# Kernel optimization log

Hardware: AMD Instinct MI355X
Metric: run time of the kernel (lower is better)

The kernel has to match this reference:

```python
import jax, jax.numpy as jnp
import numpy as np

N = 50000          # nodes
E = 400000         # edges
F = 128            # num_embeddings
NUM_TYPES = 100    # num_atoms (embedding vocab)
CUTOFF = 5.0
N_RBF = 20


def _silu(x):
    return x * jax.nn.sigmoid(x)


def setup_inputs() -> dict:
    key = jax.random.key(0)
    ks = jax.random.split(key, 16)
    pos = jax.random.normal(ks[0], (N, 3), dtype=jnp.float32) * 3.0
    z = jax.random.randint(ks[1], (N,), 0, NUM_TYPES)
    dst = jax.random.randint(ks[2], (E,), 0, N)
    # ensure src != dst so distances are nonzero
    src = (dst + 1 + jax.random.randint(ks[3], (E,), 0, N - 1)) % N
    def lin(k, fan_in, fan_out):
        kw, kb = jax.random.split(k)
        lim = 1.0 / np.sqrt(fan_in)
        W = jax.random.uniform(kw, (fan_out, fan_in), minval=-lim, maxval=lim, dtype=jnp.float32)
        b = jax.random.uniform(kb, (fan_out,), minval=-lim, maxval=lim, dtype=jnp.float32)
        return W, b
    emb_table = jax.random.normal(ks[4], (NUM_TYPES, F), dtype=jnp.float32)
    Wp1, bp1 = lin(ks[5], F, F)
    Wp2, bp2 = lin(ks[6], F, 3 * F)
    Ww, bw = lin(ks[7], N_RBF, 3 * F)
    Wu, bu = lin(ks[8], F, F)
    Wv, bv = lin(ks[9], F, F)
    Wu1, bu1 = lin(ks[10], 2 * F, F)
    Wu2, bu2 = lin(ks[11], F, 3 * F)
    return dict(pos=pos, emb_table=emb_table,
                Wp1=Wp1, bp1=bp1, Wp2=Wp2, bp2=bp2, Ww=Ww, bw=bw,
                Wu=Wu, bu=bu, Wv=Wv, bv=bv, Wu1=Wu1, bu1=bu1, Wu2=Wu2, bu2=bu2,
                z=z, src=src, dst=dst)


def painn_forward(pos, emb_table, Wp1, bp1, Wp2, bp2, Ww, bw, Wu, bu, Wv, bv,
                  Wu1, bu1, Wu2, bu2, z, src, dst):
    s = emb_table[z]                                  # [N,F] scalar features
    v = jnp.zeros((N, F, 3), dtype=s.dtype)          # equivariant features

    # ---- message block ----
    phi = _silu(s @ Wp1.T + bp1) @ Wp2.T + bp2       # [N,3F]
    rel = pos[dst] - pos[src]                        # [E,3]
    d = jnp.maximum(jnp.linalg.norm(rel, axis=-1), 1e-9)  # [E]
    n = jnp.arange(1, N_RBF + 1, dtype=jnp.float32)
    rbf = jnp.sin(n * jnp.pi * d[:, None] / CUTOFF) / d[:, None]   # [E,20]
    Wf = rbf @ Ww.T + bw                             # [E,3F]
    split = phi[src] * Wf                            # [E,3F] gated message
    ds = jax.ops.segment_sum(split[:, :F], dst, num_segments=N)    # [N,F]
    direction = rel / d[:, None]                     # [E,3]
    dv_e = v[src] * split[:, F:2 * F, None] + split[:, 2 * F:, None] * direction[:, None, :]  # [E,F,3]
    dv = jax.ops.segment_sum(dv_e, dst, num_segments=N)            # [N,F,3]
    s = s + ds
    v = v + dv

    # ---- update block ----
    U = jnp.einsum('nfc,gf->ngc', v, Wu) + bu[:, None]   # [N,F,3]
    V = jnp.einsum('nfc,gf->ngc', v, Wv) + bv[:, None]   # [N,F,3]
    Vn = jnp.linalg.norm(V, axis=-1)                     # [N,F]
    h = jnp.concatenate([s, Vn], axis=-1)                # [N,2F]
    a = _silu(h @ Wu1.T + bu1) @ Wu2.T + bu2             # [N,3F]
    dv2 = U * a[:, :F, None]                             # [N,F,3]
    ds2 = a[:, F:2 * F] + jnp.sum(U * V, axis=-1) * a[:, 2 * F:]   # [N,F]
    return s + ds2, v + dv2


def reference(pos, emb_table, Wp1, bp1, Wp2, bp2, Ww, bw, Wu, bu, Wv, bv,
              Wu1, bu1, Wu2, bu2, z, src, dst):
    return painn_forward(pos, emb_table, Wp1, bp1, Wp2, bp2, Ww, bw, Wu, bu,
                         Wv, bv, Wu1, bu1, Wu2, bu2, z, src, dst)
```

## Files before the change

kernel.cpp:

```cpp
#include <hip/hip_runtime.h>

#define NN 50000
#define EE 400000
#define FF 128
#define NRBF 20
#define MAXDEG 64
#define PI_OVER_CUT 0.6283185307179586f

typedef _Float16 h8 __attribute__((ext_vector_type(8)));
typedef float    f4 __attribute__((ext_vector_type(4)));

__global__ __launch_bounds__(256) void k_zero(int* __restrict__ counts) {
    int i = blockIdx.x * 256 + threadIdx.x;
    if (i < NN) counts[i] = 0;
}

__global__ __launch_bounds__(256) void k_bucket(const int* __restrict__ dst,
                                                int* __restrict__ counts,
                                                int* __restrict__ slots) {
    int e = blockIdx.x * 256 + threadIdx.x;
    if (e < EE) {
        int n = dst[e];
        int slot = atomicAdd(&counts[n], 1);
        if (slot < MAXDEG) slots[n * MAXDEG + slot] = e;
    }
}

__global__ __launch_bounds__(256) void k_wconv(
    const float* __restrict__ Wu, const float* __restrict__ Wv,
    const float* __restrict__ Wu1, const float* __restrict__ Wu2,
    const float* __restrict__ Wp1, const float* __restrict__ Wp2,
    _Float16* __restrict__ Wuh, _Float16* __restrict__ Wvh,
    _Float16* __restrict__ Wu1h, _Float16* __restrict__ Wu2h,
    _Float16* __restrict__ Wp1h, _Float16* __restrict__ Wp2h)
{
    int i = blockIdx.x * 256 + threadIdx.x;
    if (i < 16384) { Wuh[i] = (_Float16)Wu[i]; Wvh[i] = (_Float16)Wv[i];
                     Wp1h[i] = (_Float16)Wp1[i]; }
    if (i < 32768) { Wu1h[i] = (_Float16)Wu1[i]; }
    if (i < 49152) { Wu2h[i] = (_Float16)Wu2[i]; Wp2h[i] = (_Float16)Wp2[i]; }
}

__global__ __launch_bounds__(256) void k_node_phi_mfma(
    const float* __restrict__ emb, const int* __restrict__ z,
    const _Float16* __restrict__ Wp1h, const float* __restrict__ bp1,
    const _Float16* __restrict__ Wp2h, const float* __restrict__ bp2,
    _Float16* __restrict__ phi_s, _Float16* __restrict__ phi_v,
    float* __restrict__ s_io)
{
    __shared__ _Float16 Ss[32 * 128];
    __shared__ _Float16 H1s[32 * 128];

    const int t    = threadIdx.x;
    const int lane = t & 63;
    const int w    = t >> 6;
    const int lr   = lane & 15;
    const int lq   = lane >> 4;
    const int n0   = blockIdx.x * 32;
    const f4 z4 = {0.f, 0.f, 0.f, 0.f};

    for (int i = t; i < 512; i += 256) {
        int n = i >> 4, gr = i & 15;
        int nn = n0 + n; if (nn > NN - 1) nn = NN - 1;
        const float* sp = &emb[(size_t)z[nn] * FF + gr * 8];
        float4 aa = *(const float4*)sp;
        float4 bb = *(const float4*)(sp + 4);
        h8 hv;
        hv[0] = (_Float16)aa.x; hv[1] = (_Float16)aa.y;
        hv[2] = (_Float16)aa.z; hv[3] = (_Float16)aa.w;
        hv[4] = (_Float16)bb.x; hv[5] = (_Float16)bb.y;
        hv[6] = (_Float16)bb.z; hv[7] = (_Float16)bb.w;
        *(h8*)&Ss[(n * 16 + (gr ^ (n & 15))) * 8] = hv;
        float* op = &s_io[(size_t)nn * FF + gr * 8];
        *(float4*)op       = aa;
        *(float4*)(op + 4) = bb;
    }
    __syncthreads();

    f4 acc1[2][2];
    #pragma unroll
    for (int a = 0; a < 2; ++a)
        #pragma unroll
        for (int m = 0; m < 2; ++m) acc1[a][m] = z4;
    {
        const _Float16* bb = Wp1h + (size_t)lr * 128 + lq * 8;
        #pragma unroll
        for (int g2 = 0; g2 < 2; ++g2) {
            h8 bf[4];
            #pragma unroll
            for (int ks = 0; ks < 4; ++ks)
                bf[ks] = *(const h8*)(bb + ((2 * w + g2) * 16) * 128 + ks * 32);
            #pragma unroll
            for (int mt = 0; mt < 2; ++mt) {
                const int r = mt * 16 + lr;
                #pragma unroll
                for (int ks = 0; ks < 4; ++ks) {
                    h8 af = *(const h8*)&Ss[(r * 16 + ((ks * 4 + lq) ^ (r & 15))) * 8];
                    acc1[g2][mt] = __builtin_amdgcn_mfma_f32_16x16x32_f16(
                        af, bf[ks], acc1[g2][mt], 0, 0, 0);
                }
            }
        }
    }
    #pragma unroll
    for (int g2 = 0; g2 < 2; ++g2) {
        const int g = (2 * w + g2) * 16 + lr;
        const float b1 = bp1[g];
        #pragma unroll
        for (int mt = 0; mt < 2; ++mt)
            #pragma unroll
            for (int r = 0; r < 4; ++r) {
                float x = acc1[g2][mt][r] + b1;
                float y = x / (1.f + __expf(-x));
                int n = mt * 16 + lq * 4 + r;
                H1s[(n * 16 + ((g >> 3) ^ (n & 15))) * 8 + (g & 7)] = (_Float16)y;
            }
    }
    __syncthreads();

    f4 accS[2][2], accV[2][2];
    #pragma unroll
    for (int a = 0; a < 2; ++a)
        #pragma unroll
        for (int m = 0; m < 2; ++m) { accS[a][m] = z4; accV[a][m] = z4; }
    {
        const _Float16* bbs = Wp2h + (size_t)lr * 128 + lq * 8;
        const _Float16* bbv = Wp2h + (size_t)(256 + lr) * 128 + lq * 8;
        #pragma unroll
        for (int g2 = 0; g2 < 2; ++g2) {
            h8 bfs[4], bfv[4];
            #pragma unroll
            for (int ks = 0; ks < 4; ++ks) {
                bfs[ks] = *(const h8*)(bbs + ((2 * w + g2) * 16) * 128 + ks * 32);
                bfv[ks] = *(const h8*)(bbv + ((2 * w + g2) * 16) * 128 + ks * 32);
            }
            #pragma unroll
            for (int mt = 0; mt < 2; ++mt) {
                const int r = mt * 16 + lr;
                #pragma unroll
                for (int ks = 0; ks < 4; ++ks) {
                    h8 af = *(const h8*)&H1s[(r * 16 + ((ks * 4 + lq) ^ (r & 15))) * 8];
                    accS[g2][mt] = __builtin_amdgcn_mfma_f32_16x16x32_f16(
                        af, bfs[ks], accS[g2][mt], 0, 0, 0);
                    accV[g2][mt] = __builtin_amdgcn_mfma_f32_16x16x32_f16(
                        af, bfv[ks], accV[g2][mt], 0, 0, 0);
                }
            }
        }
    }
    #pragma unroll
    for (int g2 = 0; g2 < 2; ++g2) {
        const int g = (2 * w + g2) * 16 + lr;
        const float bsa = bp2[g], bva = bp2[256 + g];
        #pragma unroll
        for (int mt = 0; mt < 2; ++mt)
            #pragma unroll
            for (int r = 0; r < 4; ++r) {
                int n = mt * 16 + lq * 4 + r;
                int nn = n0 + n;
                if (nn < NN) {
                    size_t gi = (size_t)nn * FF + g;
                    phi_s[gi] = (_Float16)(accS[g2][mt][r] + bsa);
                    phi_v[gi] = (_Float16)(accV[g2][mt][r] + bva);
                }
            }
    }
}

__global__ __launch_bounds__(128) void k_edge(
    const float* __restrict__ pos,
    const float* __restrict__ Ww, const float* __restrict__ bw,
    const int* __restrict__ src,
    const int* __restrict__ counts, const int* __restrict__ slots,
    const _Float16* __restrict__ phi_s, const _Float16* __restrict__ phi_v,
    float* __restrict__ s_io, float* __restrict__ v_io,
    _Float16* __restrict__ xg)
{
    const int n = blockIdx.x;
    const int f = threadIdx.x;
    const int lane = threadIdx.x & 63;

    float ww_s[NRBF], ww_v[NRBF];
    #pragma unroll
    for (int k = 0; k < NRBF; k++) {
        ww_s[k] = Ww[f * NRBF + k];
        ww_v[k] = Ww[(256 + f) * NRBF + k];
    }
    const float bws = bw[f], bwv = bw[256 + f];
    const float px = pos[3 * n], py = pos[3 * n + 1], pz = pos[3 * n + 2];

    float acc_s = 0.f, av0 = 0.f, av1 = 0.f, av2 = 0.f;
    int deg = counts[n];
    deg = deg > MAXDEG ? MAXDEG : deg;

    for (int i = 0; i < deg; i++) {
        int e  = slots[n * MAXDEG + i];
        int sI = src[e];
        float rx = px - pos[3 * sI];
        float ry = py - pos[3 * sI + 1];
        float rz = pz - pos[3 * sI + 2];
        float d = sqrtf(rx * rx + ry * ry + rz * rz);
        d = fmaxf(d, 1e-9f);
        float dinv = 1.f / d;
        int kk = lane < NRBF ? lane : (NRBF - 1);
        float rbf_l = __sinf((float)(kk + 1) * PI_OVER_CUT * d) * dinv;
        int rbf_i = __float_as_int(rbf_l);
        float wfs = bws, wfv = bwv;
        #pragma unroll
        for (int k = 0; k < NRBF; k++) {
            float rk = __int_as_float(__builtin_amdgcn_readlane(rbf_i, k));
            wfs = fmaf(ww_s[k], rk, wfs);
            wfv = fmaf(ww_v[k], rk, wfv);
        }
        float sp_s = (float)phi_s[(size_t)sI * FF + f] * wfs;
        float sp_v = (float)phi_v[(size_t)sI * FF + f] * wfv;
        acc_s += sp_s;
        av0 = fmaf(sp_v, rx * dinv, av0);
        av1 = fmaf(sp_v, ry * dinv, av1);
        av2 = fmaf(sp_v, rz * dinv, av2);
    }
    size_t gi = (size_t)n * FF + f;
    s_io[gi] += acc_s;
    v_io[gi * 3 + 0] = av0;
    v_io[gi * 3 + 1] = av1;
    v_io[gi * 3 + 2] = av2;
    xg[((size_t)n * 3 + 0) * FF + f] = (_Float16)av0;
    xg[((size_t)n * 3 + 1) * FF + f] = (_Float16)av1;
    xg[((size_t)n * 3 + 2) * FF + f] = (_Float16)av2;
}

__global__ __launch_bounds__(256) void k_update_mfma(
    const _Float16* __restrict__ xg,
    const _Float16* __restrict__ Wuh, const _Float16* __restrict__ Wvh,
    const _Float16* __restrict__ Wu1h, const _Float16* __restrict__ Wu2h,
    const float* __restrict__ bu, const float* __restrict__ bv,
    const float* __restrict__ bu1, const float* __restrict__ bu2,
    float* __restrict__ s_io, float* __restrict__ v_io)
{
    __shared__ _Float16 Xs[96 * 128];
    __shared__ _Float16 Hs[32 * 256];
    __shared__ _Float16 H1s[32 * 128];

    const int t    = threadIdx.x;
    const int lane = t & 63;
    const int w    = t >> 6;
    const int lr   = lane & 15;
    const int lq   = lane >> 4;
    const int n0   = blockIdx.x * 32;
    const f4 z4 = {0.f, 0.f, 0.f, 0.f};

    for (int i = t; i < 1536; i += 256) {
        int row = i >> 4, gr = i & 15;
        int n = row & 31, c = row >> 5;
        int nn = n0 + n; if (nn > NN - 1) nn = NN - 1;
        uint4 d = *(const uint4*)&xg[((size_t)nn * 3 + c) * FF + gr * 8];
        *(uint4*)&Xs[(row * 16 + (gr ^ (row & 15))) * 8] = d;
    }
    for (int i = t; i < 512; i += 256) {
        int n = i >> 4, gr = i & 15;
        int nn = n0 + n; if (nn > NN - 1) nn = NN - 1;
        const float* sp = &s_io[(size_t)nn * FF + gr * 8];
        float4 aa = *(const float4*)sp;
        float4 bb = *(const float4*)(sp + 4);
        h8 hv;
        hv[0] = (_Float16)aa.x; hv[1] = (_Float16)aa.y;
        hv[2] = (_Float16)aa.z; hv[3] = (_Float16)aa.w;
        hv[4] = (_Float16)bb.x; hv[5] = (_Float16)bb.y;
        hv[6] = (_Float16)bb.z; hv[7] = (_Float16)bb.w;
        *(h8*)&Hs[(n * 32 + (gr ^ (n & 15))) * 8] = hv;
    }
    __syncthreads();

    f4 accU[2][6], accV[2][6];
    #pragma unroll
    for (int a = 0; a < 2; ++a)
        #pragma unroll
        for (int m = 0; m < 6; ++m) { accU[a][m] = z4; accV[a][m] = z4; }

    {
        const _Float16* bb = Wuh + (size_t)lr * 128 + lq * 8;
        h8 bf[2][4];
        #pragma unroll
        for (int g2 = 0; g2 < 2; ++g2)
            #pragma unroll
            for (int ks = 0; ks < 4; ++ks)
                bf[g2][ks] = *(const h8*)(bb + ((2 * w + g2) * 16) * 128 + ks * 32);
        #pragma unroll
        for (int mt = 0; mt < 6; ++mt) {
            const int r = mt * 16 + lr;
            h8 af[4];
            #pragma unroll
            for (int ks = 0; ks < 4; ++ks)
                af[ks] = *(const h8*)&Xs[(r * 16 + ((ks * 4 + lq) ^ (r & 15))) * 8];
            #pragma unroll
            for (int g2 = 0; g2 < 2; ++g2)
                #pragma unroll
                for (int ks = 0; ks < 4; ++ks)
                    accU[g2][mt] = __builtin_amdgcn_mfma_f32_16x16x32_f16(
                        af[ks], bf[g2][ks], accU[g2][mt], 0, 0, 0);
        }
    }
    {
        const _Float16* bb = Wvh + (size_t)lr * 128 + lq * 8;
        h8 bf[2][4];
        #pragma unroll
        for (int g2 = 0; g2 < 2; ++g2)
            #pragma unroll
            for (int ks = 0; ks < 4; ++ks)
                bf[g2][ks] = *(const h8*)(bb + ((2 * w + g2) * 16) * 128 + ks * 32);
        #pragma unroll
        for (int mt = 0; mt < 6; ++mt) {
            const int r = mt * 16 + lr;
            h8 af[4];
            #pragma unroll
            for (int ks = 0; ks < 4; ++ks)
                af[ks] = *(const h8*)&Xs[(r * 16 + ((ks * 4 + lq) ^ (r & 15))) * 8];
            #pragma unroll
            for (int g2 = 0; g2 < 2; ++g2)
                #pragma unroll
                for (int ks = 0; ks < 4; ++ks)
                    accV[g2][mt] = __builtin_amdgcn_mfma_f32_16x16x32_f16(
                        af[ks], bf[g2][ks], accV[g2][mt], 0, 0, 0);
        }
    }

    float uvr[2][2][4];
    #pragma unroll
    for (int g2 = 0; g2 < 2; ++g2) {
        const int g = (2 * w + g2) * 16 + lr;
        const float bU = bu[g], bV = bv[g];
        #pragma unroll
        for (int p = 0; p < 2; ++p) {
            #pragma unroll
            for (int r = 0; r < 4; ++r) {
                float Ux = accU[g2][0 + p][r] + bU;
                float Uy = accU[g2][2 + p][r] + bU;
                float Uz = accU[g2][4 + p][r] + bU;
                float Vx = accV[g2][0 + p][r] + bV;
                float Vy = accV[g2][2 + p][r] + bV;
                float Vz = accV[g2][4 + p][r] + bV;
                accU[g2][0 + p][r] = Ux;
                accU[g2][2 + p][r] = Uy;
                accU[g2][4 + p][r] = Uz;
                uvr[g2][p][r] = Ux * Vx + Uy * Vy + Uz * Vz;
                float vn = sqrtf(Vx * Vx + Vy * Vy + Vz * Vz);
                int n = p * 16 + lq * 4 + r;
                int gr = 16 + (g >> 3);
                Hs[(n * 32 + (gr ^ (n & 15))) * 8 + (g & 7)] = (_Float16)vn;
            }
        }
    }
    __syncthreads();

    f4 acc2[2][2];
    #pragma unroll
    for (int a = 0; a < 2; ++a)
        #pragma unroll
        for (int m = 0; m < 2; ++m) acc2[a][m] = z4;
    {
        const _Float16* bb = Wu1h + (size_t)lr * 256 + lq * 8;
        #pragma unroll
        for (int g2 = 0; g2 < 2; ++g2) {
            h8 bf[8];
            #pragma unroll
            for (int ks = 0; ks < 8; ++ks)
                bf[ks] = *(const h8*)(bb + ((2 * w + g2) * 16) * 256 + ks * 32);
            #pragma unroll
            for (int mt = 0; mt < 2; ++mt) {
                const int r = mt * 16 + lr;
                #pragma unroll
                for (int ks = 0; ks < 8; ++ks) {
                    h8 af = *(const h8*)&Hs[(r * 32 + ((ks * 4 + lq) ^ (r & 15))) * 8];
                    acc2[g2][mt] = __builtin_amdgcn_mfma_f32_16x16x32_f16(
                        af, bf[ks], acc2[g2][mt], 0, 0, 0);
                }
            }
        }
    }
    #pragma unroll
    for (int g2 = 0; g2 < 2; ++g2) {
        const int g = (2 * w + g2) * 16 + lr;
        const float b1 = bu1[g];
        #pragma unroll
        for (int mt = 0; mt < 2; ++mt)
            #pragma unroll
            for (int r = 0; r < 4; ++r) {
                float x = acc2[g2][mt][r] + b1;
                float y = x / (1.f + __expf(-x));
                int n = mt * 16 + lq * 4 + r;
                int gr = g >> 3;
                H1s[(n * 16 + (gr ^ (n & 15))) * 8 + (g & 7)] = (_Float16)y;
            }
    }
    __syncthreads();

    f4 acc3[3][2][2];
    #pragma unroll
    for (int a = 0; a < 3; ++a)
        #pragma unroll
        for (int b = 0; b < 2; ++b)
            #pragma unroll
            for (int m = 0; m < 2; ++m) acc3[a][b][m] = z4;
    {
        const _Float16* bb = Wu2h + (size_t)lr * 128 + lq * 8;
        #pragma unroll
        for (int ai = 0; ai < 3; ++ai)
            #pragma unroll
            for (int g2 = 0; g2 < 2; ++g2) {
                const int jt = ai * 8 + 2 * w + g2;
                h8 bf[4];
                #pragma unroll
                for (int ks = 0; ks < 4; ++ks)
                    bf[ks] = *(const h8*)(bb + (size_t)(jt * 16) * 128 + ks * 32);
                #pragma unroll
                for (int mt = 0; mt < 2; ++mt) {
                    const int r = mt * 16 + lr;
                    #pragma unroll
                    for (int ks = 0; ks < 4; ++ks) {
                        h8 af = *(const h8*)&H1s[(r * 16 + ((ks * 4 + lq) ^ (r & 15))) * 8];
                        acc3[ai][g2][mt] = __builtin_amdgcn_mfma_f32_16x16x32_f16(
                            af, bf[ks], acc3[ai][g2][mt], 0, 0, 0);
                    }
                }
            }
    }

    #pragma unroll
    for (int g2 = 0; g2 < 2; ++g2) {
        const int g = (2 * w + g2) * 16 + lr;
        const float b1 = bu2[g], b2 = bu2[128 + g], b3 = bu2[256 + g];
        #pragma unroll
        for (int p = 0; p < 2; ++p)
            #pragma unroll
            for (int r = 0; r < 4; ++r) {
                int n = p * 16 + lq * 4 + r;
                int nn = n0 + n;
                if (nn < NN) {
                    float a1 = acc3[0][g2][p][r] + b1;
                    float a2 = acc3[1][g2][p][r] + b2;
                    float a3 = acc3[2][g2][p][r] + b3;
                    size_t gi = (size_t)nn * FF + g;
                    s_io[gi] += a2 + uvr[g2][p][r] * a3;
                    v_io[gi * 3 + 0] += accU[g2][0 + p][r] * a1;
                    v_io[gi * 3 + 1] += accU[g2][2 + p][r] * a1;
                    v_io[gi * 3 + 2] += accU[g2][4 + p][r] * a1;
                }
            }
    }
}

extern "C" void kernel_launch(void* const* d_in, const int* in_sizes, int n_in,
                              void* d_out, int out_size, void* d_ws, size_t ws_size,
                              hipStream_t stream)
{
    const float* pos = (const float*)d_in[0];
    const float* emb = (const float*)d_in[1];
    const float* Wp1 = (const float*)d_in[2];
    const float* bp1 = (const float*)d_in[3];
    const float* Wp2 = (const float*)d_in[4];
    const float* bp2 = (const float*)d_in[5];
    const float* Ww  = (const float*)d_in[6];
    const float* bw  = (const float*)d_in[7];
    const float* Wu  = (const float*)d_in[8];
    const float* bu  = (const float*)d_in[9];
    const float* Wv  = (const float*)d_in[10];
    const float* bv  = (const float*)d_in[11];
    const float* Wu1 = (const float*)d_in[12];
    const float* bu1 = (const float*)d_in[13];
    const float* Wu2 = (const float*)d_in[14];
    const float* bu2 = (const float*)d_in[15];
    const int* z   = (const int*)d_in[16];
    const int* src = (const int*)d_in[17];
    const int* dst = (const int*)d_in[18];

    float* s_io = (float*)d_out;
    float* v_io = (float*)d_out + (size_t)NN * FF;

    char* ws = (char*)d_ws;
    _Float16* phi_s = (_Float16*)ws;
    _Float16* phi_v = phi_s + (size_t)NN * FF;
    _Float16* xg    = phi_v + (size_t)NN * FF;
    _Float16* Wuh   = xg + (size_t)NN * 3 * FF;
    _Float16* Wvh   = Wuh  + 128 * 128;
    _Float16* Wu1h  = Wvh  + 128 * 128;
    _Float16* Wu2h  = Wu1h + 128 * 256;
    _Float16* Wp1h  = Wu2h + 384 * 128;
    _Float16* Wp2h  = Wp1h + 128 * 128;
    int* counts = (int*)(Wp2h + 384 * 128);
    int* slots  = counts + NN;

    k_zero  <<<(NN + 255) / 256, 256, 0, stream>>>(counts);
    k_bucket<<<(EE + 255) / 256, 256, 0, stream>>>(dst, counts, slots);
    k_wconv <<<192, 256, 0, stream>>>(Wu, Wv, Wu1, Wu2, Wp1, Wp2,
                                      Wuh, Wvh, Wu1h, Wu2h, Wp1h, Wp2h);
    k_node_phi_mfma<<<(NN + 31) / 32, 256, 0, stream>>>(emb, z, Wp1h, bp1,
                                                        Wp2h, bp2,
                                                        phi_s, phi_v, s_io);
    k_edge<<<NN, 128, 0, stream>>>(pos, Ww, bw, src, counts, slots,
                                   phi_s, phi_v, s_io, v_io, xg);
    k_update_mfma<<<(NN + 31) / 32, 256, 0, stream>>>(xg, Wuh, Wvh, Wu1h, Wu2h,
                                                      bu, bv, bu1, bu2, s_io, v_io);
}
```

Measured before the change: 465.7 us.

## Compute edge RBF filter with MFMA and pack phi_s/phi_v into one word

The per-edge RBF→filter projection (20-wide dot products per feature, done with readlane FMAs) now runs on MFMA. Edges are batched 16 at a time into a shared A tile that carries the RBF values, a bias column set to 1 and zero padding. The weights and bias are pre-converted to a padded fp16 32-wide layout. phi_s and phi_v are stored interleaved as packed half2 so each edge needs one 32-bit gather. In exchange the filter values are rounded to fp16, and several block syncs are added per 16-edge tile, which is costly for low-degree nodes (about 8 edges on average).

New measurement: 424.9 us. 1.1x faster.

```diff
diff --git a/kernel.cpp b/kernel.cpp
--- a/kernel.cpp
+++ b/kernel.cpp
@@ -9,6 +9,8 @@
 
 typedef _Float16 h8 __attribute__((ext_vector_type(8)));
 typedef float    f4 __attribute__((ext_vector_type(4)));
+
+union pk32 { unsigned int u; _Float16 h[2]; };
 
 __global__ __launch_bounds__(256) void k_zero(int* __restrict__ counts) {
     int i = blockIdx.x * 256 + threadIdx.x;
@@ -30,23 +32,32 @@
     const float* __restrict__ Wu, const float* __restrict__ Wv,
     const float* __restrict__ Wu1, const float* __restrict__ Wu2,
     const float* __restrict__ Wp1, const float* __restrict__ Wp2,
+    const float* __restrict__ Ww, const float* __restrict__ bw,
     _Float16* __restrict__ Wuh, _Float16* __restrict__ Wvh,
     _Float16* __restrict__ Wu1h, _Float16* __restrict__ Wu2h,
-    _Float16* __restrict__ Wp1h, _Float16* __restrict__ Wp2h)
+    _Float16* __restrict__ Wp1h, _Float16* __restrict__ Wp2h,
+    _Float16* __restrict__ Wwh32)
 {
     int i = blockIdx.x * 256 + threadIdx.x;
     if (i < 16384) { Wuh[i] = (_Float16)Wu[i]; Wvh[i] = (_Float16)Wv[i];
                      Wp1h[i] = (_Float16)Wp1[i]; }
     if (i < 32768) { Wu1h[i] = (_Float16)Wu1[i]; }
     if (i < 49152) { Wu2h[i] = (_Float16)Wu2[i]; Wp2h[i] = (_Float16)Wp2[i]; }
+    if (i < 8192) {
+        int col = i >> 5, k = i & 31;
+        int sr = col < 128 ? col : col + 128;
+        _Float16 v = (_Float16)0.f;
+        if (k < 20)       v = (_Float16)Ww[sr * NRBF + k];
+        else if (k == 20) v = (_Float16)bw[sr];
+        Wwh32[i] = v;
+    }
 }
 
 __global__ __launch_bounds__(256) void k_node_phi_mfma(
     const float* __restrict__ emb, const int* __restrict__ z,
     const _Float16* __restrict__ Wp1h, const float* __restrict__ bp1,
     const _Float16* __restrict__ Wp2h, const float* __restrict__ bp2,
-    _Float16* __restrict__ phi_s, _Float16* __restrict__ phi_v,
-    float* __restrict__ s_io)
+    unsigned int* __restrict__ phi_pk, float* __restrict__ s_io)
 {
     __shared__ _Float16 Ss[32 * 128];
     __shared__ _Float16 H1s[32 * 128];
@@ -159,74 +170,122 @@
                 int n = mt * 16 + lq * 4 + r;
                 int nn = n0 + n;
                 if (nn < NN) {
-                    size_t gi = (size_t)nn * FF + g;
-                    phi_s[gi] = (_Float16)(accS[g2][mt][r] + bsa);
-                    phi_v[gi] = (_Float16)(accV[g2][mt][r] + bva);
-                }
-            }
-    }
-}
-
-__global__ __launch_bounds__(128) void k_edge(
+                    pk32 pk;
+                    pk.h[0] = (_Float16)(accS[g2][mt][r] + bsa);
+                    pk.h[1] = (_Float16)(accV[g2][mt][r] + bva);
+                    phi_pk[(size_t)nn * FF + g] = pk.u;
+                }
+            }
+    }
+}
+
+__global__ __launch_bounds__(128) void k_edge_mfma(
     const float* __restrict__ pos,
-    const float* __restrict__ Ww, const float* __restrict__ bw,
+    const _Float16* __restrict__ Wwh32,
     const int* __restrict__ src,
     const int* __restrict__ counts, const int* __restrict__ slots,
-    const _Float16* __restrict__ phi_s, const _Float16* __restrict__ phi_v,
+    const unsigned int* __restrict__ phi_pk,
     float* __restrict__ s_io, float* __restrict__ v_io,
     _Float16* __restrict__ xg)
 {
-    const int n = blockIdx.x;
-    const int f = threadIdx.x;
-    const int lane = threadIdx.x & 63;
-
-    float ww_s[NRBF], ww_v[NRBF];
-    #pragma unroll
-    for (int k = 0; k < NRBF; k++) {
-        ww_s[k] = Ww[f * NRBF + k];
-        ww_v[k] = Ww[(256 + f) * NRBF + k];
-    }
-    const float bws = bw[f], bwv = bw[256 + f];
+    __shared__ _Float16 A[16 * 32];
+    __shared__ float dirs[16][4];
+    __shared__ float dls[16];
+    __shared__ unsigned int wf[16 * 130];
+
+    const int t    = threadIdx.x;
+    const int lane = t & 63;
+    const int w    = t >> 6;
+    const int lr   = lane & 15;
+    const int lq   = lane >> 4;
+    const int n    = blockIdx.x;
+    const f4 z4 = {0.f, 0.f, 0.f, 0.f};
+
+    h8 bf[8];
+    #pragma unroll
+    for (int j = 0; j < 8; ++j)
+        bf[j] = *(const h8*)&Wwh32[(size_t)((w * 8 + j) * 16 + lr) * 32 + lq * 8];
+
     const float px = pos[3 * n], py = pos[3 * n + 1], pz = pos[3 * n + 2];
 
-    float acc_s = 0.f, av0 = 0.f, av1 = 0.f, av2 = 0.f;
     int deg = counts[n];
     deg = deg > MAXDEG ? MAXDEG : deg;
 
-    for (int i = 0; i < deg; i++) {
-        int e  = slots[n * MAXDEG + i];
-        int sI = src[e];
-        float rx = px - pos[3 * sI];
-        float ry = py - pos[3 * sI + 1];
-        float rz = pz - pos[3 * sI + 2];
-        float d = sqrtf(rx * rx + ry * ry + rz * rz);
-        d = fmaxf(d, 1e-9f);
-        float dinv = 1.f / d;
-        int kk = lane < NRBF ? lane : (NRBF - 1);
-        float rbf_l = __sinf((float)(kk + 1) * PI_OVER_CUT * d) * dinv;
-        int rbf_i = __float_as_int(rbf_l);
-        float wfs = bws, wfv = bwv;
-        #pragma unroll
-        for (int k = 0; k < NRBF; k++) {
-            float rk = __int_as_float(__builtin_amdgcn_readlane(rbf_i, k));
-            wfs = fmaf(ww_s[k], rk, wfs);
-            wfv = fmaf(ww_v[k], rk, wfv);
-        }
-        float sp_s = (float)phi_s[(size_t)sI * FF + f] * wfs;
-        float sp_v = (float)phi_v[(size_t)sI * FF + f] * wfv;
-        acc_s += sp_s;
-        av0 = fmaf(sp_v, rx * dinv, av0);
-        av1 = fmaf(sp_v, ry * dinv, av1);
-        av2 = fmaf(sp_v, rz * dinv, av2);
-    }
-    size_t gi = (size_t)n * FF + f;
+    float acc_s = 0.f, av0 = 0.f, av1 = 0.f, av2 = 0.f;
+
+    for (int t0 = 0; t0 < deg; t0 += 16) {
+        const int degT = (deg - t0) < 16 ? (deg - t0) : 16;
+        __syncthreads();
+        if (t < degT) {
+            int e  = slots[n * MAXDEG + t0 + t];
+            int sI = src[e];
+            float rx = px - pos[3 * sI];
+            float ry = py - pos[3 * sI + 1];
+            float rz = pz - pos[3 * sI + 2];
+            float d = sqrtf(rx * rx + ry * ry + rz * rz);
+            d = fmaxf(d, 1e-9f);
+            float di = 1.f / d;
+            dirs[t][0] = rx * di;
+            dirs[t][1] = ry * di;
+            dirs[t][2] = rz * di;
+            dirs[t][3] = __int_as_float(sI);
+            dls[t] = d;
+        }
+        __syncthreads();
+        {
+            const int m = t & 15, kk = t >> 4;
+            float d  = dls[m];
+            float di = 1.f / d;
+            float v0 = __sinf((float)(kk + 1) * PI_OVER_CUT * d) * di;
+            float v1 = __sinf((float)(kk + 9) * PI_OVER_CUT * d) * di;
+            float v2;
+            if (kk < 4)       v2 = __sinf((float)(kk + 17) * PI_OVER_CUT * d) * di;
+            else if (kk == 4) v2 = 1.0f;
+            else              v2 = 0.f;
+            #define STO(K, V) A[m * 32 + (((K) >> 3) ^ (m & 3)) * 8 + ((K) & 7)] = (_Float16)(V)
+            STO(kk,      v0);
+            STO(kk + 8,  v1);
+            STO(kk + 16, v2);
+            STO(kk + 24, 0.f);
+            #undef STO
+        }
+        __syncthreads();
+        {
+            h8 af = *(const h8*)&A[(lr * 4 + (lq ^ (lr & 3))) * 8];
+            #pragma unroll
+            for (int j = 0; j < 8; ++j) {
+                f4 dd = __builtin_amdgcn_mfma_f32_16x16x32_f16(af, bf[j], z4, 0, 0, 0);
+                #pragma unroll
+                for (int r = 0; r < 4; ++r) {
+                    int m = lq * 4 + r;
+                    ((_Float16*)&wf[m * 130 + j * 16 + lr])[w] = (_Float16)dd[r];
+                }
+            }
+        }
+        __syncthreads();
+        for (int m = 0; m < degT; ++m) {
+            float4 dir = *(const float4*)&dirs[m][0];
+            int sI = __builtin_amdgcn_readfirstlane(__float_as_int(dir.w));
+            pk32 ph, wfu;
+            ph.u  = phi_pk[(size_t)sI * FF + t];
+            wfu.u = wf[m * 130 + t];
+            float ps = (float)ph.h[0] * (float)wfu.h[0];
+            float pv = (float)ph.h[1] * (float)wfu.h[1];
+            acc_s += ps;
+            av0 = fmaf(pv, dir.x, av0);
+            av1 = fmaf(pv, dir.y, av1);
+            av2 = fmaf(pv, dir.z, av2);
+        }
+    }
+
+    size_t gi = (size_t)n * FF + t;
     s_io[gi] += acc_s;
     v_io[gi * 3 + 0] = av0;
     v_io[gi * 3 + 1] = av1;
     v_io[gi * 3 + 2] = av2;
-    xg[((size_t)n * 3 + 0) * FF + f] = (_Float16)av0;
-    xg[((size_t)n * 3 + 1) * FF + f] = (_Float16)av1;
-    xg[((size_t)n * 3 + 2) * FF + f] = (_Float16)av2;
+    xg[((size_t)n * 3 + 0) * FF + t] = (_Float16)av0;
+    xg[((size_t)n * 3 + 1) * FF + t] = (_Float16)av1;
+    xg[((size_t)n * 3 + 2) * FF + t] = (_Float16)av2;
 }
 
 __global__ __launch_bounds__(256) void k_update_mfma(
@@ -279,12 +338,12 @@
 
     {
         const _Float16* bb = Wuh + (size_t)lr * 128 + lq * 8;
-        h8 bf[2][4];
+        h8 bfr[2][4];
         #pragma unroll
         for (int g2 = 0; g2 < 2; ++g2)
             #pragma unroll
             for (int ks = 0; ks < 4; ++ks)
-                bf[g2][ks] = *(const h8*)(bb + ((2 * w + g2) * 16) * 128 + ks * 32);
+                bfr[g2][ks] = *(const h8*)(bb + ((2 * w + g2) * 16) * 128 + ks * 32);
         #pragma unroll
         for (int mt = 0; mt < 6; ++mt) {
             const int r = mt * 16 + lr;
@@ -297,17 +356,17 @@
                 #pragma unroll
                 for (int ks = 0; ks < 4; ++ks)
                     accU[g2][mt] = __builtin_amdgcn_mfma_f32_16x16x32_f16(
-                        af[ks], bf[g2][ks], accU[g2][mt], 0, 0, 0);
+                        af[ks], bfr[g2][ks], accU[g2][mt], 0, 0, 0);
         }
     }
     {
         const _Float16* bb = Wvh + (size_t)lr * 128 + lq * 8;
-        h8 bf[2][4];
+        h8 bfr[2][4];
         #pragma unroll
         for (int g2 = 0; g2 < 2; ++g2)
             #pragma unroll
             for (int ks = 0; ks < 4; ++ks)
-                bf[g2][ks] = *(const h8*)(bb + ((2 * w + g2) * 16) * 128 + ks * 32);
+                bfr[g2][ks] = *(const h8*)(bb + ((2 * w + g2) * 16) * 128 + ks * 32);
         #pragma unroll
         for (int mt = 0; mt < 6; ++mt) {
             const int r = mt * 16 + lr;
@@ -320,7 +379,7 @@
                 #pragma unroll
                 for (int ks = 0; ks < 4; ++ks)
                     accV[g2][mt] = __builtin_amdgcn_mfma_f32_16x16x32_f16(
-                        af[ks], bf[g2][ks], accV[g2][mt], 0, 0, 0);
+                        af[ks], bfr[g2][ks], accV[g2][mt], 0, 0, 0);
         }
     }
 
@@ -361,10 +420,10 @@
         const _Float16* bb = Wu1h + (size_t)lr * 256 + lq * 8;
         #pragma unroll
         for (int g2 = 0; g2 < 2; ++g2) {
-            h8 bf[8];
+            h8 bfr[8];
             #pragma unroll
             for (int ks = 0; ks < 8; ++ks)
-                bf[ks] = *(const h8*)(bb + ((2 * w + g2) * 16) * 256 + ks * 32);
+                bfr[ks] = *(const h8*)(bb + ((2 * w + g2) * 16) * 256 + ks * 32);
             #pragma unroll
             for (int mt = 0; mt < 2; ++mt) {
                 const int r = mt * 16 + lr;
@@ -372,7 +431,7 @@
                 for (int ks = 0; ks < 8; ++ks) {
                     h8 af = *(const h8*)&Hs[(r * 32 + ((ks * 4 + lq) ^ (r & 15))) * 8];
                     acc2[g2][mt] = __builtin_amdgcn_mfma_f32_16x16x32_f16(
-                        af, bf[ks], acc2[g2][mt], 0, 0, 0);
+                        af, bfr[ks], acc2[g2][mt], 0, 0, 0);
                 }
             }
         }
@@ -408,10 +467,10 @@
             #pragma unroll
             for (int g2 = 0; g2 < 2; ++g2) {
                 const int jt = ai * 8 + 2 * w + g2;
-                h8 bf[4];
+                h8 bfr[4];
                 #pragma unroll
                 for (int ks = 0; ks < 4; ++ks)
-                    bf[ks] = *(const h8*)(bb + (size_t)(jt * 16) * 128 + ks * 32);
+                    bfr[ks] = *(const h8*)(bb + (size_t)(jt * 16) * 128 + ks * 32);
                 #pragma unroll
                 for (int mt = 0; mt < 2; ++mt) {
                     const int r = mt * 16 + lr;
@@ -419,7 +478,7 @@
                     for (int ks = 0; ks < 4; ++ks) {
                         h8 af = *(const h8*)&H1s[(r * 16 + ((ks * 4 + lq) ^ (r & 15))) * 8];
                         acc3[ai][g2][mt] = __builtin_amdgcn_mfma_f32_16x16x32_f16(
-                            af, bf[ks], acc3[ai][g2][mt], 0, 0, 0);
+                            af, bfr[ks], acc3[ai][g2][mt], 0, 0, 0);
                     }
                 }
             }
@@ -477,27 +536,27 @@
     float* v_io = (float*)d_out + (size_t)NN * FF;
 
     char* ws = (char*)d_ws;
-    _Float16* phi_s = (_Float16*)ws;
-    _Float16* phi_v = phi_s + (size_t)NN * FF;
-    _Float16* xg    = phi_v + (size_t)NN * FF;
+    unsigned int* phi_pk = (unsigned int*)ws;
+    _Float16* xg    = (_Float16*)(phi_pk + (size_t)NN * FF);
     _Float16* Wuh   = xg + (size_t)NN * 3 * FF;
     _Float16* Wvh   = Wuh  + 128 * 128;
     _Float16* Wu1h  = Wvh  + 128 * 128;
     _Float16* Wu2h  = Wu1h + 128 * 256;
     _Float16* Wp1h  = Wu2h + 384 * 128;
     _Float16* Wp2h  = Wp1h + 128 * 128;
-    int* counts = (int*)(Wp2h + 384 * 128);
+    _Float16* Wwh32 = Wp2h + 384 * 128;
+    int* counts = (int*)(Wwh32 + 256 * 32);
     int* slots  = counts + NN;
 
     k_zero  <<<(NN + 255) / 256, 256, 0, stream>>>(counts);
     k_bucket<<<(EE + 255) / 256, 256, 0, stream>>>(dst, counts, slots);
-    k_wconv <<<192, 256, 0, stream>>>(Wu, Wv, Wu1, Wu2, Wp1, Wp2,
-                                      Wuh, Wvh, Wu1h, Wu2h, Wp1h, Wp2h);
+    k_wconv <<<192, 256, 0, stream>>>(Wu, Wv, Wu1, Wu2, Wp1, Wp2, Ww, bw,
+                                      Wuh, Wvh, Wu1h, Wu2h, Wp1h, Wp2h, Wwh32);
     k_node_phi_mfma<<<(NN + 31) / 32, 256, 0, stream>>>(emb, z, Wp1h, bp1,
                                                         Wp2h, bp2,
-                                                        phi_s, phi_v, s_io);
-    k_edge<<<NN, 128, 0, stream>>>(pos, Ww, bw, src, counts, slots,
-                                   phi_s, phi_v, s_io, v_io, xg);
+                                                        phi_pk, s_io);
+    k_edge_mfma<<<NN, 128, 0, stream>>>(pos, Wwh32, src, counts, slots,
+                                        phi_pk, s_io, v_io, xg);
     k_update_mfma<<<(NN + 31) / 32, 256, 0, stream>>>(xg, Wuh, Wvh, Wu1h, Wu2h,
                                                       bu, bv, bu1, bu2, s_io, v_io);
 }
```
